# Optimization experiments

Measured on AMD Instinct MI355X. Metric: run time of the kernel, lower is better.

## Reference

```python
import jax, jax.numpy as jnp
import numpy as np


def setup_inputs() -> dict:
    key = jax.random.key(0)
    k = jax.random.split(key, 6)
    BS, T, ZCH, H, W = 16, 8, 256, 16, 16
    VOCAB, EMB = 4096, 256
    x = jax.random.uniform(k[0], (BS, T, ZCH, H, W), dtype=jnp.float32)
    # Embedding init mirrors uniform_(-1/vocab, 1/vocab)
    codebook = jax.random.uniform(k[1], (VOCAB, EMB), dtype=jnp.float32,
                                  minval=-1.0 / VOCAB, maxval=1.0 / VOCAB)
    pre_w = jax.random.normal(k[2], (EMB, ZCH), dtype=jnp.float32) * 0.02
    pre_b = jax.random.normal(k[3], (EMB,), dtype=jnp.float32) * 0.02
    post_w = jax.random.normal(k[4], (ZCH, EMB), dtype=jnp.float32) * 0.02
    post_b = jax.random.normal(k[5], (ZCH,), dtype=jnp.float32) * 0.02
    return {"x": x, "codebook": codebook, "pre_w": pre_w, "pre_b": pre_b,
            "post_w": post_w, "post_b": post_b}


def reference(x, codebook, pre_w, pre_b, post_w, post_b):
    bs, t, zch, h, w = x.shape
    vocab, emb = codebook.shape
    # preprocess: [0,1] -> [-1,1]
    xp = x * 2.0 - 1.0
    # flatten time into batch; encoder is identity (external module)
    z_in = xp.reshape(bs * t, zch, h, w)
    # pre_quantize_conv: 1x1 conv == per-pixel linear (z_ch -> emb)
    z = jnp.einsum('bchw,ec->behw', z_in, pre_w) + pre_b[None, :, None, None]
    # flatten: (b h w) e  -- matches rearrange('b e h w -> (b h w) e')
    zf = z.transpose(0, 2, 3, 1).reshape(-1, emb)  # [N, emb]
    # squared cdist via expansion: ||z||^2 + ||c||^2 - 2 z.c
    z_sq = jnp.sum(zf * zf, axis=-1, keepdims=True)          # [N,1]
    c_sq = jnp.sum(codebook * codebook, axis=-1)             # [V]
    dist = z_sq + c_sq[None, :] - 2.0 * (zf @ codebook.T)    # [N,V]
    tokens = jnp.argmin(dist, axis=-1)                        # [N]
    zq = codebook[tokens]                                     # [N, emb] gather
    zq = zq.reshape(bs * t, h, w, emb).transpose(0, 3, 1, 2)  # b e h w
    # straight-through estimator
    dec_in = z + jax.lax.stop_gradient(zq - z)
    # post_quantize_conv: 1x1 conv (emb -> z_ch); decoder is identity
    recon = jnp.einsum('behw,ce->bchw', dec_in, post_w) + post_b[None, :, None, None]
    z_out = z.reshape(bs, t, emb, h, w)
    zq_out = zq.reshape(bs, t, emb, h, w)
    recon_out = recon.reshape(bs, t, zch, h, w)
    tokens_out = tokens.reshape(bs, t, h * w)
    return z_out, zq_out, recon_out, tokens_out
```

## Files before the change

### kernel.cpp

```cpp
#include <hip/hip_runtime.h>
#include <float.h>
#include <stdint.h>

#define BB   128
#define CCH  256
#define EMB_ 256
#define HW   256
#define NPIX 32768
#define VOC  4096

typedef _Float16 f16x8 __attribute__((ext_vector_type(8)));
typedef float    f32x4 __attribute__((ext_vector_type(4)));

__device__ __forceinline__ void async16(void* lds, const void* g) {
    __builtin_amdgcn_global_load_lds((const __attribute__((address_space(1))) uint32_t*)g,
                                     (__attribute__((address_space(3))) uint32_t*)lds,
                                     16, 0, 0);
}

__global__ __launch_bounds__(256) void k_prep(const float* __restrict__ cb,
                                              const float* __restrict__ post_w,
                                              const float* __restrict__ post_b,
                                              const float* __restrict__ pre_w,
                                              float* __restrict__ postcode,
                                              _Float16* __restrict__ B3,
                                              float* __restrict__ csq,
                                              _Float16* __restrict__ W3) {
    __shared__ float smem[4352];
    const int bid = blockIdx.x;
    const int tid = threadIdx.x;

    if (bid < 256) {
        float (*cbs)[EMB_] = (float(*)[EMB_])smem;
        int v0 = bid * 16;
        int c  = tid;
#pragma unroll
        for (int r = 0; r < 16; ++r)
            cbs[r][c] = cb[(v0 + r) * EMB_ + c];
        __syncthreads();
        float acc[16];
        float bias = post_b[c];
#pragma unroll
        for (int r = 0; r < 16; ++r) acc[r] = bias;
        const float4* w4p = (const float4*)(post_w + c * EMB_);
        for (int e4 = 0; e4 < 64; ++e4) {
            float4 w4 = w4p[e4];
#pragma unroll
            for (int r = 0; r < 16; ++r) {
                float4 c4 = *(const float4*)&cbs[r][e4 * 4];
                acc[r] = fmaf(w4.x, c4.x, fmaf(w4.y, c4.y,
                         fmaf(w4.z, c4.z, fmaf(w4.w, c4.w, acc[r]))));
            }
        }
#pragma unroll
        for (int r = 0; r < 16; ++r)
            postcode[(v0 + r) * CCH + c] = acc[r];
    } else if (bid < 512) {
        float (*cs)[17] = (float(*)[17])smem;
        int vg = bid - 256;
        int vr = tid >> 4, e0 = (tid & 15) << 4;
        const float* cp = cb + (vg * 16 + vr) * EMB_ + e0;
#pragma unroll
        for (int j = 0; j < 16; ++j)
            cs[e0 + j][vr] = cp[j];
        __syncthreads();
#pragma unroll
        for (int it = 0; it < 4; ++it) {
            int c = it * 256 + tid;
            int kc8 = c >> 4, row = c & 15;
            int lo = kc8 >> 5;
            int kh = kc8 & 31;
            f16x8 outv;
#pragma unroll
            for (int j = 0; j < 8; ++j) {
                float v = cs[kh * 8 + j][row] * 65536.0f;
                _Float16 h = (_Float16)v;
                if (lo) h = (_Float16)(v - (float)h);
                outv[j] = h;
            }
            *(f16x8*)(B3 + ((vg * 64 + kc8) * 128 + row * 8)) = outv;
        }
    } else if (bid < 528) {
        int v = (bid - 512) * 256 + tid;
        const float4* row = (const float4*)(cb + v * EMB_);
        float s = 0.f;
#pragma unroll 8
        for (int q = 0; q < 64; ++q) {
            float4 a = row[q];
            s = fmaf(a.x, a.x, fmaf(a.y, a.y, fmaf(a.z, a.z, fmaf(a.w, a.w, s))));
        }
        csq[v] = s;
    } else {
        int eg = bid - 528;
#pragma unroll
        for (int i = 0; i < 4; ++i) {
            int flat = i * 256 + tid;
            int u = flat >> 4, row = flat & 15;
            int part = u >> 5, c8 = u & 31;
            const float* wp = pre_w + (eg * 16 + row) * CCH + c8 * 8;
            f16x8 outv;
#pragma unroll
            for (int j = 0; j < 8; ++j) {
                float v = wp[j] * 16.0f;
                _Float16 h = (_Float16)v;
                if (part) h = (_Float16)((v - (float)h) * 4096.0f);
                outv[j] = h;
            }
            *(f16x8*)(W3 + ((eg * 64 + u) * 128 + row * 8)) = outv;
        }
    }
}

__global__ __launch_bounds__(512) void k_zgemm(const float* __restrict__ x,
                                               const _Float16* __restrict__ W3,
                                               const float* __restrict__ pre_b,
                                               float* __restrict__ zout,
                                               _Float16* __restrict__ A3) {
    __shared__ __align__(16) char smem[99328];
    float* pbs = (float*)(smem + 98304);

    const int tid = threadIdx.x;
    const int l   = tid & 63;
    const int w   = tid >> 6;
    const int l15 = l & 15, l4 = l >> 4;
    const int wr  = w >> 2, wc = w & 3;
    const int bM  = blockIdx.x;
    const int b   = bM >> 1, hw0 = (bM & 1) * 128;

    const int xng = tid >> 6, xu = (tid >> 4) & 3, xrow = tid & 15;
    const float* xbase = x + (size_t)b * (CCH * HW) + hw0 + xng * 16 + xrow;

#define STAGE_W(CC, BUF) {                                                   \
    _Pragma("unroll")                                                        \
    for (int i = 0; i < 2; ++i) {                                            \
        int flat = i * 512 + tid; int eg = flat >> 6, sub = flat & 63;       \
        async16((_Float16*)(smem + (BUF) * 16384) + flat * 8,                \
                W3 + (eg * 64 + (CC) * 4) * 128 + sub * 8);                  \
        async16((_Float16*)(smem + 32768 + (BUF) * 16384) + flat * 8,        \
                W3 + (eg * 64 + 32 + (CC) * 4) * 128 + sub * 8);             \
    } }

#define STAGE_X(CC, BUF) {                                                   \
    const float* xp_ = xbase + ((CC) * 32 + xu * 8) * HW;                    \
    f16x8 hv, lv;                                                            \
    _Pragma("unroll")                                                        \
    for (int j = 0; j < 8; ++j) {                                            \
        float xv = 2.0f * xp_[j * HW] - 1.0f;                     \
        _Float16 h = (_Float16)xv;                                           \
        lv[j] = (_Float16)((xv - (float)h) * 4096.0f);   \
        hv[j] = h;                                                           \
    }                                                                        \
    *(f16x8*)((_Float16*)(smem + 65536 + (BUF) * 8192) + tid * 8) = hv;      \
    *(f16x8*)((_Float16*)(smem + 81920 + (BUF) * 8192) + tid * 8) = lv;      \
    }

    if (tid < 256) pbs[tid] = pre_b[tid];
    STAGE_W(0, 0)
    STAGE_X(0, 0)
    __syncthreads();

    f32x4 accA[4][4], accB[4][4];
    const f32x4 zero4 = {0.f, 0.f, 0.f, 0.f};
#pragma unroll
    for (int m = 0; m < 4; ++m)
#pragma unroll
        for (int s = 0; s < 4; ++s) { accA[m][s] = zero4; accB[m][s] = zero4; }

    int buf = 0;
    for (int cc = 0; cc < 8; ++cc) {
        if (cc < 7) { STAGE_W(cc + 1, buf ^ 1) STAGE_X(cc + 1, buf ^ 1) }
        const _Float16* WhC = (const _Float16*)(smem + buf * 16384);
        const _Float16* WlC = (const _Float16*)(smem + 32768 + buf * 16384);
        const _Float16* XhC = (const _Float16*)(smem + 65536 + buf * 8192);
        const _Float16* XlC = (const _Float16*)(smem + 81920 + buf * 8192);
        f16x8 whf[4], wlf[4], xhf[4], xlf[4];
#pragma unroll
        for (int m = 0; m < 4; ++m) {
            whf[m] = *(const f16x8*)&WhC[((wc * 4 + m) * 64 + l4 * 16 + l15) * 8];
            wlf[m] = *(const f16x8*)&WlC[((wc * 4 + m) * 64 + l4 * 16 + l15) * 8];
        }
#pragma unroll
        for (int s = 0; s < 4; ++s) {
            xhf[s] = *(const f16x8*)&XhC[((wr * 4 + s) * 64 + l4 * 16 + l15) * 8];
            xlf[s] = *(const f16x8*)&XlC[((wr * 4 + s) * 64 + l4 * 16 + l15) * 8];
        }
#pragma unroll
        for (int m = 0; m < 4; ++m)
#pragma unroll
            for (int s = 0; s < 4; ++s)
                accA[m][s] = __builtin_amdgcn_mfma_f32_16x16x32_f16(whf[m], xhf[s], accA[m][s], 0, 0, 0);
#pragma unroll
        for (int m = 0; m < 4; ++m)
#pragma unroll
            for (int s = 0; s < 4; ++s)
                accB[m][s] = __builtin_amdgcn_mfma_f32_16x16x32_f16(whf[m], xlf[s], accB[m][s], 0, 0, 0);
#pragma unroll
        for (int m = 0; m < 4; ++m)
#pragma unroll
            for (int s = 0; s < 4; ++s)
                accB[m][s] = __builtin_amdgcn_mfma_f32_16x16x32_f16(wlf[m], xhf[s], accB[m][s], 0, 0, 0);
        __syncthreads();
        buf ^= 1;
    }

    float* zw = (float*)(smem + w * 5120);
    const size_t zbase = (size_t)b * (EMB_ * HW) + hw0;
#pragma unroll
    for (int m = 0; m < 4; ++m) {
        asm volatile("s_waitcnt lgkmcnt(0)" ::: "memory");
        __builtin_amdgcn_sched_barrier(0);
        f32x4 zv[4];
#pragma unroll
        for (int s = 0; s < 4; ++s) {
#pragma unroll
            for (int r = 0; r < 4; ++r) {
                float g = fmaf(accB[m][s][r], 0x1p-12f, accA[m][s][r]) * 0x1p-4f;
                zv[s][r] = g + pbs[wc * 64 + m * 16 + l4 * 4 + r];
            }
            *(f32x4*)(zw + (s * 16 + l15) * 20 + l4 * 4) = zv[s];
#pragma unroll
            for (int r = 0; r < 4; ++r)
                zout[zbase + (size_t)(wc * 64 + m * 16 + l4 * 4 + r) * HW
                     + wr * 64 + s * 16 + l15] = zv[s][r];
        }
        asm volatile("s_waitcnt lgkmcnt(0)" ::: "memory");
        __builtin_amdgcn_sched_barrier(0);
#pragma unroll
        for (int o = 0; o < 4; ++o) {
            int flat = o * 64 + l;
            int part = flat >> 7, rest = flat & 127;
            int pg = rest >> 5, uq = (rest >> 4) & 1, row = rest & 15;
            int nloc = pg * 16 + row;
            float4 va = *(const float4*)(zw + nloc * 20 + uq * 8);
            float4 vb = *(const float4*)(zw + nloc * 20 + uq * 8 + 4);
            float vs[8] = {va.x, va.y, va.z, va.w, vb.x, vb.y, vb.z, vb.w};
            f16x8 outv;
#pragma unroll
            for (int j = 0; j < 8; ++j) {
                float v = vs[j] * 256.0f;
                _Float16 h = (_Float16)v;
                if (part) h = (_Float16)(v - (float)h);
                outv[j] = h;
            }
            *(f16x8*)(A3 + ((size_t)(bM * 8 + wr * 4 + pg) * 64
                            + part * 32 + wc * 8 + m * 2 + uq) * 128 + row * 8) = outv;
        }
    }
#undef STAGE_W
#undef STAGE_X
}

__device__ __forceinline__ void issueA(const _Float16* __restrict__ A3, int bM,
                                       int w, int l, _Float16* dst, int kA) {
#pragma unroll
    for (int i = 0; i < 2; ++i) {
        int pg = 2 * w + i;
        const _Float16* g = A3 + ((bM * 16 + pg) * 64 + kA) * 128 + l * 8;
        async16(dst + pg * 512, g);
    }
}

__device__ __forceinline__ void issueB(const _Float16* __restrict__ B3, int vgbase,
                                       int w, int l, _Float16* dst, int kB) {
#pragma unroll
    for (int i = 0; i < 2; ++i) {
        int vg = 2 * w + i;
        const _Float16* g = B3 + ((vgbase + vg) * 64 + kB) * 128 + l * 8;
        async16(dst + vg * 512, g);
    }
}

__global__ __launch_bounds__(512) void k_dist(const float* __restrict__ zout,
                                              const _Float16* __restrict__ A3,
                                              const _Float16* __restrict__ B3,
                                              const float* __restrict__ csq,
                                              float* __restrict__ bestw,
                                              int* __restrict__ bidxw) {
    __shared__ __align__(16) _Float16 Ab[4][8192];
    __shared__ __align__(16) _Float16 Bb[4][8192];
    __shared__ float csq_s[2048];
    __shared__ float zsq_s[256];
    __shared__ float red_b[8][128];
    __shared__ int   red_i[8][128];

    const int tid = threadIdx.x;
    const int l   = tid & 63;
    const int w   = tid >> 6;
    const int l15 = l & 15, l4 = l >> 4;
    const int wr  = w >> 2, wc = w & 3;
    const int bM  = blockIdx.x & 127;
    const int nh  = blockIdx.x >> 7;
    const int vgb = nh * 128;

    issueA(A3, bM, w, l, Ab[0], 0);  issueB(B3, vgb, w, l, Bb[0], 0);
    issueA(A3, bM, w, l, Ab[1], 4);  issueB(B3, vgb, w, l, Bb[1], 4);
    issueA(A3, bM, w, l, Ab[2], 8);  issueB(B3, vgb, w, l, Bb[2], 8);

#pragma unroll
    for (int j = 0; j < 4; ++j) csq_s[j * 512 + tid] = csq[nh * 2048 + j * 512 + tid];

    if (tid < 256) {
        const float* zp = zout + bM * (EMB_ * HW) + tid;
        float s = 0.f;
        for (int k = 0; k < 256; ++k) { float zv = zp[k * HW]; s = fmaf(zv, zv, s); }
        zsq_s[tid] = s;
    }
    __syncthreads();

    float best[32]; int bidx[32];
#pragma unroll
    for (int i = 0; i < 32; ++i) { best[i] = FLT_MAX; bidx[i] = 0; }

    const f32x4 zero4 = {0.f, 0.f, 0.f, 0.f};
    int cur = 0;
    for (int vt = 0; vt < 8; ++vt) {
        f32x4 acc[8][4];
#pragma unroll
        for (int s = 0; s < 8; ++s)
#pragma unroll
            for (int m = 0; m < 4; ++m) acc[s][m] = zero4;

        for (int kc = 0; kc < 24; ++kc) {
            const int n = vt * 24 + kc;
            int kc3 = kc + 3, vt3 = vt;
            if (kc3 >= 24) { kc3 -= 24; ++vt3; }
            const int nxt = (cur + 3) & 3;
            const bool pf = (vt3 < 8);
            const int kA3 = ((kc3 >= 16) ? 32 : 0) + (kc3 & 7) * 4;
            const int kB3 = ((kc3 >= 8 && kc3 < 16) ? 32 : 0) + (kc3 & 7) * 4;

            f16x8 af0[4], bf[4];
#pragma unroll
            for (int s = 0; s < 4; ++s)
                af0[s] = *(const f16x8*)&Ab[cur][(wr * 8 + s) * 512 + l4 * 128 + l15 * 8];
#pragma unroll
            for (int m = 0; m < 4; ++m)
                bf[m] = *(const f16x8*)&Bb[cur][(wc * 4 + m) * 512 + l4 * 128 + l15 * 8];
            if (pf) issueA(A3, bM, w, l, Ab[nxt], kA3);
            __builtin_amdgcn_s_barrier();
            asm volatile("s_waitcnt lgkmcnt(0)" ::: "memory");
            __builtin_amdgcn_sched_barrier(0);
            __builtin_amdgcn_s_setprio(1);
#pragma unroll
            for (int s = 0; s < 4; ++s)
#pragma unroll
                for (int m = 0; m < 4; ++m)
                    acc[s][m] = __builtin_amdgcn_mfma_f32_16x16x32_f16(af0[s], bf[m], acc[s][m], 0, 0, 0);
            __builtin_amdgcn_s_setprio(0);
            __builtin_amdgcn_s_barrier();

            f16x8 af1[4];
#pragma unroll
            for (int s = 0; s < 4; ++s)
                af1[s] = *(const f16x8*)&Ab[cur][(wr * 8 + 4 + s) * 512 + l4 * 128 + l15 * 8];
            if (pf) issueB(B3, vgb + vt3 * 16, w, l, Bb[nxt], kB3);
            __builtin_amdgcn_s_barrier();
            asm volatile("s_waitcnt lgkmcnt(0)" ::: "memory");
            __builtin_amdgcn_sched_barrier(0);
            __builtin_amdgcn_s_setprio(1);
#pragma unroll
            for (int s = 0; s < 4; ++s)
#pragma unroll
                for (int m = 0; m < 4; ++m)
                    acc[4 + s][m] = __builtin_amdgcn_mfma_f32_16x16x32_f16(af1[s], bf[m], acc[4 + s][m], 0, 0, 0);
            __builtin_amdgcn_s_setprio(0);
            if (n <= 188)      { asm volatile("s_waitcnt vmcnt(8)" ::: "memory"); }
            else if (n == 189) { asm volatile("s_waitcnt vmcnt(4)" ::: "memory"); }
            else               { asm volatile("s_waitcnt vmcnt(0)" ::: "memory"); }
            __builtin_amdgcn_s_barrier();
            __builtin_amdgcn_sched_barrier(0);
            cur = (cur + 1) & 3;
        }

#pragma unroll
        for (int m = 0; m < 4; ++m) {
            int cl = vt * 256 + (wc * 4 + m) * 16 + l15;
            float cs = csq_s[cl];
            int code = nh * 2048 + cl;
#pragma unroll
            for (int s = 0; s < 8; ++s)
#pragma unroll
                for (int r = 0; r < 4; ++r) {
                    float dd = (zsq_s[wr * 128 + s * 16 + l4 * 4 + r] + cs)
                               - acc[s][m][r] * 0x1p-23f;
                    int pi = s * 4 + r;
                    if (dd < best[pi]) { best[pi] = dd; bidx[pi] = code; }
                }
        }
    }

#pragma unroll
    for (int off = 8; off >= 1; off >>= 1) {
#pragma unroll
        for (int i = 0; i < 32; ++i) {
            float ob = __shfl_xor(best[i], off, 64);
            int   oi = __shfl_xor(bidx[i], off, 64);
            if (ob < best[i] || (ob == best[i] && oi < bidx[i])) { best[i] = ob; bidx[i] = oi; }
        }
    }
    if (l15 == 0) {
#pragma unroll
        for (int s = 0; s < 8; ++s)
#pragma unroll
            for (int r = 0; r < 4; ++r) {
                int pl = s * 16 + l4 * 4 + r;
                red_b[w][pl] = best[s * 4 + r];
                red_i[w][pl] = bidx[s * 4 + r];
            }
    }
    __syncthreads();
    if (tid < 256) {
        int wrg = tid >> 7, pl = tid & 127;
        float bb = red_b[wrg * 4][pl]; int bi = red_i[wrg * 4][pl];
#pragma unroll
        for (int c = 1; c < 4; ++c) {
            float ob = red_b[wrg * 4 + c][pl]; int oi = red_i[wrg * 4 + c][pl];
            if (ob < bb || (ob == bb && oi < bi)) { bb = ob; bi = oi; }
        }
        bestw[nh * NPIX + bM * 256 + tid] = bb;
        bidxw[nh * NPIX + bM * 256 + tid] = bi;
    }
}

__global__ __launch_bounds__(256) void k_argmin2(const float* __restrict__ bestw,
                                                 const int* __restrict__ bidxw,
                                                 float* __restrict__ tok_f) {
    int i = blockIdx.x * 256 + threadIdx.x;
    float b0 = bestw[i], b1 = bestw[NPIX + i];
    int   i0 = bidxw[i], i1 = bidxw[NPIX + i];
    tok_f[i] = (float)((b1 < b0) ? i1 : i0);
}

__global__ __launch_bounds__(256) void k_gather(const float* __restrict__ tok_f,
                                                const float* __restrict__ cb,
                                                const float* __restrict__ postcode,
                                                float* __restrict__ zq_out,
                                                float* __restrict__ recon) {
    int b  = blockIdx.x >> 3;
    int e0 = (blockIdx.x & 7) * 32;
    int hw = threadIdx.x;
    int t  = (int)tok_f[b * HW + hw];
    const float* cbr = cb       + t * EMB_;
    const float* pcr = postcode + t * CCH;
    float* zq = zq_out + b * (EMB_ * HW) + hw;
    float* rc = recon  + b * (CCH * HW) + hw;
#pragma unroll
    for (int j = 0; j < 32; ++j) {
        int e = e0 + j;
        zq[e * HW] = cbr[e];
        rc[e * HW] = pcr[e];
    }
}

__global__ __launch_bounds__(256) void k_gather2(const float* __restrict__ bestw,
                                                 const int* __restrict__ bidxw,
                                                 const float* __restrict__ cb,
                                                 const float* __restrict__ postcode,
                                                 float* __restrict__ zq_out,
                                                 float* __restrict__ recon,
                                                 float* __restrict__ tok_f) {
    __shared__ float rows[64][257];
    __shared__ int   toks[64];
    const int b    = blockIdx.x >> 1;
    const int half = blockIdx.x & 1;
    const int tid  = threadIdx.x;
    const int p    = tid & 63, eg = tid >> 6;

    for (int g = 0; g < 2; ++g) {
        int px0 = half * 128 + g * 64;
        if (tid < 64) {
            int i = b * HW + px0 + tid;
            float b0 = bestw[i], b1 = bestw[NPIX + i];
            int   i0 = bidxw[i], i1 = bidxw[NPIX + i];
            int t = (b1 < b0) ? i1 : i0;
            toks[tid] = t;
            tok_f[i] = (float)t;
        }
        __syncthreads();
#pragma unroll 8
        for (int r = 0; r < 64; ++r)
            rows[r][tid] = cb[(size_t)toks[r] * EMB_ + tid];
        __syncthreads();
        {
            float* zq = zq_out + (size_t)b * (EMB_ * HW) + px0 + p;
#pragma unroll 8
            for (int eo = 0; eo < 64; ++eo) {
                int e = eg * 64 + eo;
                zq[(size_t)e * HW] = rows[p][e];
            }
        }
        __syncthreads();
#pragma unroll 8
        for (int r = 0; r < 64; ++r)
            rows[r][tid] = postcode[(size_t)toks[r] * CCH + tid];
        __syncthreads();
        {
            float* rc = recon + (size_t)b * (CCH * HW) + px0 + p;
#pragma unroll 8
            for (int eo = 0; eo < 64; ++eo) {
                int e = eg * 64 + eo;
                rc[(size_t)e * HW] = rows[p][e];
            }
        }
        __syncthreads();
    }
}

extern "C" void kernel_launch(void* const* d_in, const int* in_sizes, int n_in,
                              void* d_out, int out_size, void* d_ws, size_t ws_size,
                              hipStream_t stream) {
    const float* x      = (const float*)d_in[0];
    const float* cb     = (const float*)d_in[1];
    const float* pre_w  = (const float*)d_in[2];
    const float* pre_b  = (const float*)d_in[3];
    const float* post_w = (const float*)d_in[4];
    const float* post_b = (const float*)d_in[5];

    float* out    = (float*)d_out;
    float* z_out  = out;
    float* zq_out = out + 8388608;
    float* recon  = out + 16777216;
    float* tok_f  = out + 25165824;

    _Float16* A3 = (_Float16*)zq_out;
    _Float16* B3 = (_Float16*)recon;
    _Float16* W3 = (_Float16*)(recon + 1048576 + 4 * NPIX);

    float* csq      = (float*)d_ws;
    float* postcode = csq + VOC;

    size_t need = (size_t)(VOC + VOC * CCH + 4 * NPIX) * sizeof(float);
    bool fused = (ws_size >= need);
    float* bestw; int* bidxw;
    if (fused) {
        bestw = postcode + (size_t)VOC * CCH;
        bidxw = (int*)(bestw + 2 * NPIX);
    } else {
        bestw = recon + 1048576;
        bidxw = (int*)(recon + 1048576 + 2 * NPIX);
    }

    k_prep <<< 544, 256, 0, stream>>>(cb, post_w, post_b, pre_w,
                                      postcode, B3, csq, W3);
    k_zgemm<<< 256, 512, 0, stream>>>(x, W3, pre_b, z_out, A3);
    k_dist <<< 256, 512, 0, stream>>>(z_out, A3, B3, csq, bestw, bidxw);
    if (fused) {
        k_gather2<<< 256, 256, 0, stream>>>(bestw, bidxw, cb, postcode,
                                            zq_out, recon, tok_f);
    } else {
        k_argmin2<<< 128, 256, 0, stream>>>(bestw, bidxw, tok_f);
        k_gather <<<1024, 256, 0, stream>>>(tok_f, cb, postcode, zq_out, recon);
    }
}
```

Baseline: 390.6 us.

## Switch k_dist to 3-stage LDS pipeline with fully unrolled k-loop

Reduces the async global-to-LDS prefetch ring in the distance kernel from 4 buffers with depth-3 prefetch to 3 buffers with depth-2. The 24-step k-loop is fully unrolled so buffer indices and offsets become compile-time constants, and the per-tile address math moves into precomputed base pointers. The argmin epilogue is reordered so the zsq values are loaded once per row group and reused across the codebook columns. This cuts LDS footprint and index arithmetic, but the shallower prefetch may expose more global-load latency, and full unrolling raises code size and register pressure.

Result: slower. 541.8 us (+38.7%).

```diff
diff --git a/kernel.cpp b/kernel.cpp
--- a/kernel.cpp
+++ b/kernel.cpp
@@ -250,34 +250,14 @@
 #undef STAGE_X
 }
 
-__device__ __forceinline__ void issueA(const _Float16* __restrict__ A3, int bM,
-                                       int w, int l, _Float16* dst, int kA) {
-#pragma unroll
-    for (int i = 0; i < 2; ++i) {
-        int pg = 2 * w + i;
-        const _Float16* g = A3 + ((bM * 16 + pg) * 64 + kA) * 128 + l * 8;
-        async16(dst + pg * 512, g);
-    }
-}
-
-__device__ __forceinline__ void issueB(const _Float16* __restrict__ B3, int vgbase,
-                                       int w, int l, _Float16* dst, int kB) {
-#pragma unroll
-    for (int i = 0; i < 2; ++i) {
-        int vg = 2 * w + i;
-        const _Float16* g = B3 + ((vgbase + vg) * 64 + kB) * 128 + l * 8;
-        async16(dst + vg * 512, g);
-    }
-}
-
 __global__ __launch_bounds__(512) void k_dist(const float* __restrict__ zout,
                                               const _Float16* __restrict__ A3,
                                               const _Float16* __restrict__ B3,
                                               const float* __restrict__ csq,
                                               float* __restrict__ bestw,
                                               int* __restrict__ bidxw) {
-    __shared__ __align__(16) _Float16 Ab[4][8192];
-    __shared__ __align__(16) _Float16 Bb[4][8192];
+    __shared__ __align__(16) _Float16 Ab[3][8192];
+    __shared__ __align__(16) _Float16 Bb[3][8192];
     __shared__ float csq_s[2048];
     __shared__ float zsq_s[256];
     __shared__ float red_b[8][128];
@@ -292,9 +272,20 @@
     const int nh  = blockIdx.x >> 7;
     const int vgb = nh * 128;
 
-    issueA(A3, bM, w, l, Ab[0], 0);  issueB(B3, vgb, w, l, Bb[0], 0);
-    issueA(A3, bM, w, l, Ab[1], 4);  issueB(B3, vgb, w, l, Bb[1], 4);
-    issueA(A3, bM, w, l, Ab[2], 8);  issueB(B3, vgb, w, l, Bb[2], 8);
+    const _Float16* gA = A3 + (size_t)(bM * 16 + 2 * w) * 8192 + l * 8;
+    const _Float16* gB = B3 + (size_t)(vgb + 2 * w) * 8192 + l * 8;
+    _Float16* dstA[3] = { Ab[0] + 2 * w * 512, Ab[1] + 2 * w * 512, Ab[2] + 2 * w * 512 };
+    _Float16* dstB[3] = { Bb[0] + 2 * w * 512, Bb[1] + 2 * w * 512, Bb[2] + 2 * w * 512 };
+    const int aoff = (wr * 8) * 512 + l4 * 128 + l15 * 8;
+    const int boff = (wc * 4) * 512 + l4 * 128 + l15 * 8;
+
+#define ISSA(BUF, KA) { async16(dstA[BUF],       gA + (KA) * 128);           \
+                        async16(dstA[BUF] + 512, gA + 8192 + (KA) * 128); }
+#define ISSB(BUF, VT2, KB) { const _Float16* gb_ = gB + (size_t)(VT2) * 131072 + (KB) * 128; \
+                        async16(dstB[BUF], gb_); async16(dstB[BUF] + 512, gb_ + 8192); }
+
+    ISSA(0, 0) ISSB(0, 0, 0)
+    ISSA(1, 4) ISSB(1, 0, 4)
 
 #pragma unroll
     for (int j = 0; j < 4; ++j) csq_s[j * 512 + tid] = csq[nh * 2048 + j * 512 + tid];
@@ -312,7 +303,6 @@
     for (int i = 0; i < 32; ++i) { best[i] = FLT_MAX; bidx[i] = 0; }
 
     const f32x4 zero4 = {0.f, 0.f, 0.f, 0.f};
-    int cur = 0;
     for (int vt = 0; vt < 8; ++vt) {
         f32x4 acc[8][4];
 #pragma unroll
@@ -320,23 +310,24 @@
 #pragma unroll
             for (int m = 0; m < 4; ++m) acc[s][m] = zero4;
 
+#pragma unroll
         for (int kc = 0; kc < 24; ++kc) {
-            const int n = vt * 24 + kc;
-            int kc3 = kc + 3, vt3 = vt;
-            if (kc3 >= 24) { kc3 -= 24; ++vt3; }
-            const int nxt = (cur + 3) & 3;
-            const bool pf = (vt3 < 8);
-            const int kA3 = ((kc3 >= 16) ? 32 : 0) + (kc3 & 7) * 4;
-            const int kB3 = ((kc3 >= 8 && kc3 < 16) ? 32 : 0) + (kc3 & 7) * 4;
+            const int CUR = kc % 3;
+            const int NXT = (kc + 2) % 3;
+            const int kc2w = (kc + 2 >= 24) ? kc - 22 : kc + 2;
+            const int kA2 = ((kc2w >= 16) ? 32 : 0) + (kc2w & 7) * 4;
+            const int kB2 = ((kc2w >= 8 && kc2w < 16) ? 32 : 0) + (kc2w & 7) * 4;
+            const bool wraps = (kc + 2 >= 24);
 
             f16x8 af0[4], bf[4];
 #pragma unroll
             for (int s = 0; s < 4; ++s)
-                af0[s] = *(const f16x8*)&Ab[cur][(wr * 8 + s) * 512 + l4 * 128 + l15 * 8];
+                af0[s] = *(const f16x8*)&Ab[CUR][aoff + s * 512];
 #pragma unroll
             for (int m = 0; m < 4; ++m)
-                bf[m] = *(const f16x8*)&Bb[cur][(wc * 4 + m) * 512 + l4 * 128 + l15 * 8];
-            if (pf) issueA(A3, bM, w, l, Ab[nxt], kA3);
+                bf[m] = *(const f16x8*)&Bb[CUR][boff + m * 512];
+            if (!wraps)           { ISSA(NXT, kA2) }
+            else if (vt < 7)      { ISSA(NXT, kA2) }
             __builtin_amdgcn_s_barrier();
             asm volatile("s_waitcnt lgkmcnt(0)" ::: "memory");
             __builtin_amdgcn_sched_barrier(0);
@@ -352,8 +343,9 @@
             f16x8 af1[4];
 #pragma unroll
             for (int s = 0; s < 4; ++s)
-                af1[s] = *(const f16x8*)&Ab[cur][(wr * 8 + 4 + s) * 512 + l4 * 128 + l15 * 8];
-            if (pf) issueB(B3, vgb + vt3 * 16, w, l, Bb[nxt], kB3);
+                af1[s] = *(const f16x8*)&Ab[CUR][aoff + (4 + s) * 512];
+            if (!wraps)           { ISSB(NXT, vt, kB2) }
+            else if (vt < 7)      { ISSB(NXT, vt + 1, kB2) }
             __builtin_amdgcn_s_barrier();
             asm volatile("s_waitcnt lgkmcnt(0)" ::: "memory");
             __builtin_amdgcn_sched_barrier(0);
@@ -364,30 +356,42 @@
                 for (int m = 0; m < 4; ++m)
                     acc[4 + s][m] = __builtin_amdgcn_mfma_f32_16x16x32_f16(af1[s], bf[m], acc[4 + s][m], 0, 0, 0);
             __builtin_amdgcn_s_setprio(0);
-            if (n <= 188)      { asm volatile("s_waitcnt vmcnt(8)" ::: "memory"); }
-            else if (n == 189) { asm volatile("s_waitcnt vmcnt(4)" ::: "memory"); }
-            else               { asm volatile("s_waitcnt vmcnt(0)" ::: "memory"); }
+            if (kc == 22) {
+                if (vt == 7) { asm volatile("s_waitcnt vmcnt(0)" ::: "memory"); }
+                else         { asm volatile("s_waitcnt vmcnt(4)" ::: "memory"); }
+            } else         { asm volatile("s_waitcnt vmcnt(4)" ::: "memory"); }
             __builtin_amdgcn_s_barrier();
             __builtin_amdgcn_sched_barrier(0);
-            cur = (cur + 1) & 3;
-        }
-
+        }
+
+        float csm[4]; int codem[4];
 #pragma unroll
         for (int m = 0; m < 4; ++m) {
             int cl = vt * 256 + (wc * 4 + m) * 16 + l15;
-            float cs = csq_s[cl];
-            int code = nh * 2048 + cl;
-#pragma unroll
-            for (int s = 0; s < 8; ++s)
-#pragma unroll
-                for (int r = 0; r < 4; ++r) {
-                    float dd = (zsq_s[wr * 128 + s * 16 + l4 * 4 + r] + cs)
-                               - acc[s][m][r] * 0x1p-23f;
-                    int pi = s * 4 + r;
-                    if (dd < best[pi]) { best[pi] = dd; bidx[pi] = code; }
-                }
-        }
-    }
+            csm[m] = csq_s[cl];
+            codem[m] = nh * 2048 + cl;
+        }
+#pragma unroll
+        for (int s = 0; s < 8; ++s) {
+            float zq0 = zsq_s[wr * 128 + s * 16 + l4 * 4 + 0];
+            float zq1 = zsq_s[wr * 128 + s * 16 + l4 * 4 + 1];
+            float zq2 = zsq_s[wr * 128 + s * 16 + l4 * 4 + 2];
+            float zq3 = zsq_s[wr * 128 + s * 16 + l4 * 4 + 3];
+#pragma unroll
+            for (int m = 0; m < 4; ++m) {
+                float dd0 = (zq0 + csm[m]) - acc[s][m][0] * 0x1p-23f;
+                float dd1 = (zq1 + csm[m]) - acc[s][m][1] * 0x1p-23f;
+                float dd2 = (zq2 + csm[m]) - acc[s][m][2] * 0x1p-23f;
+                float dd3 = (zq3 + csm[m]) - acc[s][m][3] * 0x1p-23f;
+                if (dd0 < best[s * 4 + 0]) { best[s * 4 + 0] = dd0; bidx[s * 4 + 0] = codem[m]; }
+                if (dd1 < best[s * 4 + 1]) { best[s * 4 + 1] = dd1; bidx[s * 4 + 1] = codem[m]; }
+                if (dd2 < best[s * 4 + 2]) { best[s * 4 + 2] = dd2; bidx[s * 4 + 2] = codem[m]; }
+                if (dd3 < best[s * 4 + 3]) { best[s * 4 + 3] = dd3; bidx[s * 4 + 3] = codem[m]; }
+            }
+        }
+    }
+#undef ISSA
+#undef ISSB
 
 #pragma unroll
     for (int off = 8; off >= 1; off >>= 1) {
```
